# Optimization experiments

Measured on AMD Instinct MI355X. Metric: run time of the kernel, lower is better.

Reference implementation:

```python
import jax, jax.numpy as jnp
import numpy as np

B, T, C, E = 16, 1024, 256, 512
NUM_CENTER = [512, 256, 128]
NUM_NNS = [16, 32, 64]
BN_EPS = 1e-5


def _fps(pts, K):
    # farthest point sampling, deterministic start at index 0. pts: [B,N,3] -> [B,K] int32
    N = pts.shape[1]
    def one(p):
        def step(carry, _):
            d, cur = carry
            dist = jnp.sum((p - p[cur]) ** 2, axis=-1)
            d = jnp.minimum(d, dist)
            nxt = jnp.argmax(d).astype(jnp.int32)
            return (d, nxt), cur
        init = (jnp.full((N,), jnp.inf, p.dtype), jnp.int32(0))
        _, idxs = jax.lax.scan(step, init, None, length=K)
        return idxs
    return jax.vmap(one)(pts)


def _knn(q, t, k):
    # k nearest neighbors of each query q [B,Tq,3] among targets t [B,Tt,3] -> [B,Tq,k]
    d2 = (jnp.sum(q * q, -1)[:, :, None] + jnp.sum(t * t, -1)[:, None, :]
          - 2.0 * jnp.einsum('bqc,btc->bqt', q, t))
    _, idx = jax.lax.top_k(-d2, k)
    return idx


def _gather(x, idx):
    # x [B,N,C], idx [B,M] -> [B,M,C]
    return jax.vmap(lambda xb, ib: xb[ib])(x, idx)


def _knn_gather(x, idx):
    # x [B,N,C], idx [B,M,K] -> [B,M,K,C]
    return jax.vmap(lambda xb, ib: xb[ib])(x, idx)


def _bn(x, g, b):
    # training-mode BatchNorm1d over leading (batch) dim of [N,C]
    m = jnp.mean(x, axis=0)
    v = jnp.mean((x - m) ** 2, axis=0)
    return (x - m) * jax.lax.rsqrt(v + BN_EPS) * g + b


def reference(tokens, centers, lrfs, wq, wkv, mlp_w1, mlp_b1, mlp_w2, mlp_b2,
              bn1_g, bn1_b, bn2_g, bn2_b, att_w1, att_b1, att_w2, att_b2,
              emb_w, emb_b, embn_g, embn_b):
    Bq, Tt, Cd = tokens.shape
    centers_target = centers
    lrfs_target = lrfs.reshape(Bq, Tt, 9)
    tokens_target = tokens
    T_target = Tt
    for i in range(len(NUM_CENTER)):
        Tq = NUM_CENTER[i]
        k = NUM_NNS[i]
        rep_idx = _fps(centers_target, Tq)                      # [B,Tq]
        centers_query = _gather(centers_target, rep_idx)        # [B,Tq,3]
        lrfs_query = _gather(lrfs_target, rep_idx)              # [B,Tq,9]
        tokens_query = _gather(tokens_target, rep_idx)          # [B,Tq,C]
        nn_idx = _knn(centers_query, centers_target, k)         # [B,Tq,k]
        skip = tokens_query.reshape(Bq * Tq, Cd)
        if i > 0:
            t = jnp.concatenate([tokens_query, tokens_target], axis=1)
            t = _bn(t.reshape(Bq * (Tq + T_target), Cd), bn1_g[i], bn1_b[i])
            t = t.reshape(Bq, Tq + T_target, Cd)
            tokens_query, tokens_target = t[:, :Tq, :], t[:, Tq:, :]
        Q = tokens_query @ wq[i]                                # [B,Tq,C]
        KV = tokens_target @ wkv[i]                             # [B,Tt,2C]
        Kf, Vf = KV[..., :Cd], KV[..., Cd:]
        Kn = _knn_gather(Kf, nn_idx).reshape(Bq * Tq, k, Cd)
        Vn = _knn_gather(Vf, nn_idx).reshape(Bq * Tq, k, Cd)
        Qf = Q.reshape(Bq * Tq, Cd)
        # vector self-attention: elementwise Q-K diff -> MLP -> softmax over neighbors
        diff = Qf[:, None, :] - Kn                              # [B*Tq,k,C]
        sim = jax.nn.relu(diff @ att_w1[i] + att_b1[i]) @ att_w2[i] + att_b2[i]
        A = jax.nn.softmax(sim, axis=1)
        tq = jnp.sum(A * Vn, axis=1)                            # [B*Tq,C]
        tq = tq + skip
        skip2 = tq
        tq = _bn(tq, bn2_g[i], bn2_b[i])
        tq = jax.nn.relu(tq @ mlp_w1[i] + mlp_b1[i]) @ mlp_w2[i] + mlp_b2[i]
        tq = tq + skip2
        T_target = Tq
        centers_target = centers_query
        lrfs_target = lrfs_query
        tokens_target = tq.reshape(Bq, Tq, Cd)
    g = jnp.mean(tokens_target, axis=1)                         # [B,C]
    g = jax.nn.relu(_bn(g @ emb_w + emb_b, embn_g, embn_b))     # [B,E]
    # ksparse: keep top-64 activations per row
    vals, _ = jax.lax.top_k(g, 64)
    thr = vals[:, -1:]
    g = jnp.where(g >= thr, g, 0.0)
    n = jnp.maximum(jnp.linalg.norm(g, axis=1, keepdims=True), 1e-12)
    return g / n


def setup_inputs() -> dict:
    key = jax.random.key(0)
    ks = jax.random.split(key, 10)
    s = 0.05
    return {
        'tokens': jax.random.normal(ks[0], (B, T, C), jnp.float32),
        'centers': jax.random.normal(ks[1], (B, T, 3), jnp.float32),
        'lrfs': jax.random.normal(ks[2], (B, T, 3, 3), jnp.float32),
        'wq': jax.random.normal(ks[3], (3, C, C), jnp.float32) * s,
        'wkv': jax.random.normal(ks[4], (3, C, 2 * C), jnp.float32) * s,
        'mlp_w1': jax.random.normal(ks[5], (3, C, 2 * C), jnp.float32) * s,
        'mlp_b1': jnp.zeros((3, 2 * C), jnp.float32),
        'mlp_w2': jax.random.normal(ks[6], (3, 2 * C, C), jnp.float32) * s,
        'mlp_b2': jnp.zeros((3, C), jnp.float32),
        'bn1_g': jnp.ones((3, C), jnp.float32),
        'bn1_b': jnp.zeros((3, C), jnp.float32),
        'bn2_g': jnp.ones((3, C), jnp.float32),
        'bn2_b': jnp.zeros((3, C), jnp.float32),
        'att_w1': jax.random.normal(ks[7], (3, C, C), jnp.float32) * s,
        'att_b1': jnp.zeros((3, C), jnp.float32),
        'att_w2': jax.random.normal(ks[8], (3, C, C), jnp.float32) * s,
        'att_b2': jnp.zeros((3, C), jnp.float32),
        'emb_w': jax.random.normal(ks[9], (C, E), jnp.float32) * s,
        'emb_b': jnp.zeros((E,), jnp.float32),
        'embn_g': jnp.ones((E,), jnp.float32),
        'embn_b': jnp.zeros((E,), jnp.float32),
    }
```

## Files before the change

### kernel.cpp

```cpp
#include <hip/hip_runtime.h>
#include <cstdint>
#include <cmath>

static constexpr int BB = 16;
static constexpr int TT0 = 1024;
static constexpr int CC = 256;
static constexpr int EE = 512;

typedef __bf16 bf16x8 __attribute__((ext_vector_type(8)));
typedef float  f32x4  __attribute__((ext_vector_type(4)));

template <int NPL>
__device__ void fps_body(float4* sp, const float* __restrict__ ctr,
                         int Tt, int Ksel, int* __restrict__ rep,
                         int b, int lane)
{
  const float* base = ctr + (size_t)b * Tt * 3;
  float x[NPL], y[NPL], z[NPL], d[NPL];
  #pragma unroll
  for (int j = 0; j < NPL; ++j) {
    int idx = lane * NPL + j;
    x[j] = base[idx * 3 + 0];
    y[j] = base[idx * 3 + 1];
    z[j] = base[idx * 3 + 2];
    d[j] = INFINITY;
    sp[idx] = make_float4(x[j], y[j], z[j], 0.f);
  }
  int cur = 0;
  for (int s = 0; s < Ksel; ++s) {
    if (lane == 0) rep[b * Ksel + s] = cur;
    float4 cpt = sp[cur];
    unsigned long long key = 0ull;
    #pragma unroll
    for (int j = 0; j < NPL; ++j) {
      float dx = __fsub_rn(x[j], cpt.x);
      float dy = __fsub_rn(y[j], cpt.y);
      float dz = __fsub_rn(z[j], cpt.z);
      float dist = __fadd_rn(__fadd_rn(__fmul_rn(dx, dx), __fmul_rn(dy, dy)),
                             __fmul_rn(dz, dz));
      float nd = fminf(d[j], dist);
      d[j] = nd;
      unsigned long long kj =
          ((unsigned long long)__float_as_uint(nd) << 32) |
          (unsigned)(0xFFFFFFFFu - (unsigned)(lane * NPL + j));
      key = (kj > key) ? kj : key;
    }
    float ld = __uint_as_float((unsigned)(key >> 32));
    float rm = ld;
    {
      int t;
      t = __builtin_amdgcn_mov_dpp(__float_as_int(rm), 0x121, 0xf, 0xf, false);
      rm = fmaxf(rm, __int_as_float(t));
      t = __builtin_amdgcn_mov_dpp(__float_as_int(rm), 0x122, 0xf, 0xf, false);
      rm = fmaxf(rm, __int_as_float(t));
      t = __builtin_amdgcn_mov_dpp(__float_as_int(rm), 0x124, 0xf, 0xf, false);
      rm = fmaxf(rm, __int_as_float(t));
      t = __builtin_amdgcn_mov_dpp(__float_as_int(rm), 0x128, 0xf, 0xf, false);
      rm = fmaxf(rm, __int_as_float(t));
    }
    float r0 = __uint_as_float((unsigned)__builtin_amdgcn_readlane(__float_as_int(rm), 0));
    float r1 = __uint_as_float((unsigned)__builtin_amdgcn_readlane(__float_as_int(rm), 16));
    float r2 = __uint_as_float((unsigned)__builtin_amdgcn_readlane(__float_as_int(rm), 32));
    float r3 = __uint_as_float((unsigned)__builtin_amdgcn_readlane(__float_as_int(rm), 48));
    float gm = fmaxf(fmaxf(r0, r1), fmaxf(r2, r3));
    unsigned long long mask = __ballot(ld == gm);
    int wl = __ffsll(mask) - 1;
    unsigned lowkey = (unsigned)__builtin_amdgcn_readlane((int)(unsigned)key, wl);
    cur = (int)(0xFFFFFFFFu - lowkey);
  }
}

template <int NPL2>
__global__ __launch_bounds__(256) void knn_wave_kernel(
    const float* __restrict__ cq, const float* __restrict__ ct,
    int Tq, int Tt, int Kn, int* __restrict__ nn)
{
  int wid = threadIdx.x >> 6, lane = threadIdx.x & 63;
  int r = blockIdx.x * 4 + wid;
  int b = r / Tq;
  const float* tb = ct + (size_t)b * Tt * 3;
  float qx = cq[(size_t)r * 3 + 0];
  float qy = cq[(size_t)r * 3 + 1];
  float qz = cq[(size_t)r * 3 + 2];
  float sq = __fadd_rn(__fadd_rn(__fmul_rn(qx, qx), __fmul_rn(qy, qy)),
                       __fmul_rn(qz, qz));
  unsigned long long key[NPL2];
  #pragma unroll
  for (int j = 0; j < NPL2; ++j) {
    int t = lane * NPL2 + j;
    float tx = tb[t * 3 + 0], ty = tb[t * 3 + 1], tz = tb[t * 3 + 2];
    float st = __fadd_rn(__fadd_rn(__fmul_rn(tx, tx), __fmul_rn(ty, ty)),
                         __fmul_rn(tz, tz));
    float dot = __fadd_rn(__fadd_rn(__fmul_rn(qx, tx), __fmul_rn(qy, ty)),
                          __fmul_rn(qz, tz));
    float d2 = __fsub_rn(__fadd_rn(sq, st), __fmul_rn(2.0f, dot));
    unsigned ub = __float_as_uint(d2);
    ub ^= (ub >> 31) ? 0xFFFFFFFFu : 0x80000000u;
    key[j] = ((unsigned long long)ub << 32) | (unsigned)t;
  }
  for (int k = 0; k < Kn; ++k) {
    unsigned long long lmin = ~0ull;
    #pragma unroll
    for (int j = 0; j < NPL2; ++j) lmin = (key[j] < lmin) ? key[j] : lmin;
    unsigned md = (unsigned)(lmin >> 32);
    unsigned rm = md;
    {
      unsigned t;
      t = (unsigned)__builtin_amdgcn_mov_dpp((int)rm, 0x121, 0xf, 0xf, false);
      rm = (t < rm) ? t : rm;
      t = (unsigned)__builtin_amdgcn_mov_dpp((int)rm, 0x122, 0xf, 0xf, false);
      rm = (t < rm) ? t : rm;
      t = (unsigned)__builtin_amdgcn_mov_dpp((int)rm, 0x124, 0xf, 0xf, false);
      rm = (t < rm) ? t : rm;
      t = (unsigned)__builtin_amdgcn_mov_dpp((int)rm, 0x128, 0xf, 0xf, false);
      rm = (t < rm) ? t : rm;
    }
    unsigned r0 = (unsigned)__builtin_amdgcn_readlane((int)rm, 0);
    unsigned r1 = (unsigned)__builtin_amdgcn_readlane((int)rm, 16);
    unsigned r2 = (unsigned)__builtin_amdgcn_readlane((int)rm, 32);
    unsigned r3 = (unsigned)__builtin_amdgcn_readlane((int)rm, 48);
    unsigned g01 = (r0 < r1) ? r0 : r1;
    unsigned g23 = (r2 < r3) ? r2 : r3;
    unsigned gmin = (g01 < g23) ? g01 : g23;
    unsigned long long mask = __ballot(md == gmin);
    int wl = __ffsll(mask) - 1;
    int wt = __builtin_amdgcn_readlane((int)(unsigned)lmin, wl);
    if (lane == 0) nn[(size_t)r * Kn + k] = wt;
    #pragma unroll
    for (int j = 0; j < NPL2; ++j)
      if (lane * NPL2 + j == wt) key[j] = ~0ull;
  }
}

__global__ void gather_rows_kernel(
    const float* __restrict__ src, const int* __restrict__ idx,
    float* __restrict__ dst, int Tq, int Tt, int D, int total)
{
  int i = blockIdx.x * blockDim.x + threadIdx.x;
  if (i >= total) return;
  int d = i % D;
  int q = (i / D) % Tq;
  int b = i / (D * Tq);
  int s = idx[b * Tq + q];
  dst[i] = src[((size_t)b * Tt + s) * D + d];
}

__global__ __launch_bounds__(256) void bn_stats_kernel(
    const float* __restrict__ x1, int R1, const float* __restrict__ x2, int R2,
    float* __restrict__ part, int nch)
{
  int c = threadIdx.x;
  int chunk = blockIdx.x;
  int R = R1 + R2;
  int per = (R + nch - 1) / nch;
  int r0 = chunk * per;
  int r1 = min(r0 + per, R);
  float s = 0.f, ss = 0.f;
  for (int r = r0; r < r1; ++r) {
    float v = (r < R1) ? x1[(size_t)r * 256 + c] : x2[(size_t)(r - R1) * 256 + c];
    s += v;
    ss = fmaf(v, v, ss);
  }
  part[(size_t)chunk * 512 + c] = s;
  part[(size_t)chunk * 512 + 256 + c] = ss;
}

__global__ __launch_bounds__(256) void bn_finalize_kernel(
    const float* __restrict__ part, int nch, int R,
    float* __restrict__ mean, float* __restrict__ rstd)
{
  int c = threadIdx.x;
  float s = 0.f, ss = 0.f;
  for (int k = 0; k < nch; ++k) {
    s += part[(size_t)k * 512 + c];
    ss += part[(size_t)k * 512 + 256 + c];
  }
  float m = s / (float)R;
  float v = ss / (float)R - m * m;
  if (v < 0.f) v = 0.f;
  mean[c] = m;
  rstd[c] = rsqrtf(v + 1e-5f);
}

__global__ __launch_bounds__(256) void gemm_kernel(
    const float* __restrict__ A, int lda,
    const float* __restrict__ W, int ldw,
    const float* __restrict__ bias, const float* __restrict__ resid,
    float* __restrict__ out, int M, int N, int K, int relu)
{
  __shared__ float As[32][68];
  __shared__ float Bs[32][68];
  int bm = blockIdx.y * 64;
  int bn = blockIdx.x * 64;
  int tid = threadIdx.x;
  int tx = tid & 15, ty = tid >> 4;
  int arow = tid >> 3;
  int ak = (tid & 7) * 4;
  int wk = tid >> 4;
  int wn = (tid & 15) * 4;
  float acc[4][4] = {{0.f}};
  for (int k0 = 0; k0 < K; k0 += 32) {
    #pragma unroll
    for (int h = 0; h < 2; ++h) {
      int row = bm + arow + h * 32;
      float4 a = (row < M)
          ? *(const float4*)&A[(size_t)row * lda + k0 + ak]
          : make_float4(0.f, 0.f, 0.f, 0.f);
      As[ak + 0][arow + h * 32] = a.x;
      As[ak + 1][arow + h * 32] = a.y;
      As[ak + 2][arow + h * 32] = a.z;
      As[ak + 3][arow + h * 32] = a.w;
    }
    #pragma unroll
    for (int h = 0; h < 2; ++h) {
      int krow = k0 + wk + h * 16;
      *(float4*)&Bs[wk + h * 16][wn] =
          *(const float4*)&W[(size_t)krow * ldw + bn + wn];
    }
    __syncthreads();
    #pragma unroll
    for (int k = 0; k < 32; ++k) {
      float4 a = *(const float4*)&As[k][ty * 4];
      float4 b = *(const float4*)&Bs[k][tx * 4];
      float av[4] = {a.x, a.y, a.z, a.w};
      float bv[4] = {b.x, b.y, b.z, b.w};
      #pragma unroll
      for (int i = 0; i < 4; ++i)
        #pragma unroll
        for (int j = 0; j < 4; ++j)
          acc[i][j] = fmaf(av[i], bv[j], acc[i][j]);
    }
    __syncthreads();
  }
  #pragma unroll
  for (int i = 0; i < 4; ++i) {
    int m = bm + ty * 4 + i;
    if (m >= M) continue;
    #pragma unroll
    for (int j = 0; j < 4; ++j) {
      int n = bn + tx * 4 + j;
      float v = acc[i][j];
      if (bias) v += bias[n];
      if (relu) v = fmaxf(v, 0.f);
      if (resid) v += resid[(size_t)m * N + n];
      out[(size_t)m * N + n] = v;
    }
  }
}

__global__ void splitT_kernel(
    const float* __restrict__ src, int ldw, int K, int N,
    __bf16* __restrict__ hi, __bf16* __restrict__ lo, int total)
{
  int i = blockIdx.x * blockDim.x + threadIdx.x;
  if (i >= total) return;
  int n = i / K;
  int k = i - n * K;
  float v = src[(size_t)k * ldw + n];
  __bf16 h = (__bf16)v;
  hi[i] = h;
  lo[i] = (__bf16)(v - (float)h);
}

__global__ __launch_bounds__(256) void split_w2_kernel(
    const float* __restrict__ w2, __bf16* __restrict__ hi,
    __bf16* __restrict__ lo)
{
  int i = blockIdx.x * 256 + threadIdx.x;
  int s = i >> 16;
  int e = i & 65535;
  int cp = e >> 8;
  int cc = e & 255;
  float v = w2[((size_t)s << 16) + cc * 256 + cp];
  __bf16 h = (__bf16)v;
  hi[i] = h;
  lo[i] = (__bf16)(v - (float)h);
}

template <int NPL>
__global__ __launch_bounds__(256) void gemm_mfma_kernel(
    const float* __restrict__ A, int lda,
    const __bf16* __restrict__ WThi, const __bf16* __restrict__ WTlo,
    const float* __restrict__ bias, const float* __restrict__ resid,
    float* __restrict__ out, int M, int N, int K, int relu,
    const float* __restrict__ bnm, const float* __restrict__ bnr,
    const float* __restrict__ bng, const float* __restrict__ bnb,
    int nbx,
    const float* __restrict__ fps_ctr, int fps_Tt, int fps_Ksel,
    int* __restrict__ fps_rep)
{
  __shared__ __align__(16) float As[128 * 36];
  if ((int)blockIdx.x >= nbx) {
    if (fps_rep == nullptr || (int)blockIdx.y >= BB) return;
    if ((int)threadIdx.x >= 64) return;
    fps_body<NPL>((float4*)As, fps_ctr, fps_Tt, fps_Ksel, fps_rep,
                  blockIdx.y, threadIdx.x);
    return;
  }
  int bm = blockIdx.y * 128;
  int bn = blockIdx.x * 64;
  int tid = threadIdx.x;
  int w = tid >> 6, lane = tid & 63;
  int jl = lane & 15;
  int kg = lane >> 4;

  f32x4 acc[2][4];
  #pragma unroll
  for (int mt = 0; mt < 2; ++mt)
    #pragma unroll
    for (int nt = 0; nt < 4; ++nt) acc[mt][nt] = (f32x4){0.f, 0.f, 0.f, 0.f};

  for (int k0 = 0; k0 < K; k0 += 32) {
    #pragma unroll
    for (int f = 0; f < 4; ++f) {
      int fi = tid + f * 256;
      int row = fi >> 3, c4 = fi & 7;
      float4 v = *(const float4*)&A[(size_t)(bm + row) * lda + k0 + c4 * 4];
      if (bnm) {
        int kk = k0 + c4 * 4;
        float4 m4 = *(const float4*)&bnm[kk];
        float4 r4 = *(const float4*)&bnr[kk];
        float4 g4 = *(const float4*)&bng[kk];
        float4 b4 = *(const float4*)&bnb[kk];
        v.x = (v.x - m4.x) * r4.x * g4.x + b4.x;
        v.y = (v.y - m4.y) * r4.y * g4.y + b4.y;
        v.z = (v.z - m4.z) * r4.z * g4.z + b4.z;
        v.w = (v.w - m4.w) * r4.w * g4.w + b4.w;
      }
      *(float4*)&As[row * 36 + c4 * 4] = v;
    }
    __syncthreads();
    bf16x8 ahi[2], alo[2];
    #pragma unroll
    for (int mt = 0; mt < 2; ++mt) {
      int row = (w * 2 + mt) * 16 + jl;
      float4 a0 = *(const float4*)&As[row * 36 + kg * 8];
      float4 a1 = *(const float4*)&As[row * 36 + kg * 8 + 4];
      float hv[8] = {a0.x, a0.y, a0.z, a0.w, a1.x, a1.y, a1.z, a1.w};
      #pragma unroll
      for (int i = 0; i < 8; ++i) {
        __bf16 t0 = (__bf16)hv[i];
        ahi[mt][i] = t0;
        alo[mt][i] = (__bf16)(hv[i] - (float)t0);
      }
    }
    #pragma unroll
    for (int nt = 0; nt < 4; ++nt) {
      size_t boff = (size_t)(bn + nt * 16 + jl) * K + k0 + kg * 8;
      bf16x8 bhi = *(const bf16x8*)(WThi + boff);
      bf16x8 blo = *(const bf16x8*)(WTlo + boff);
      #pragma unroll
      for (int mt = 0; mt < 2; ++mt) {
        acc[mt][nt] = __builtin_amdgcn_mfma_f32_16x16x32_bf16(alo[mt], bhi, acc[mt][nt], 0, 0, 0);
        acc[mt][nt] = __builtin_amdgcn_mfma_f32_16x16x32_bf16(ahi[mt], blo, acc[mt][nt], 0, 0, 0);
        acc[mt][nt] = __builtin_amdgcn_mfma_f32_16x16x32_bf16(ahi[mt], bhi, acc[mt][nt], 0, 0, 0);
      }
    }
    __syncthreads();
  }
  #pragma unroll
  for (int mt = 0; mt < 2; ++mt)
    #pragma unroll
    for (int nt = 0; nt < 4; ++nt)
      #pragma unroll
      for (int qi = 0; qi < 4; ++qi) {
        int m = bm + (w * 2 + mt) * 16 + kg * 4 + qi;
        int n = bn + nt * 16 + jl;
        float v = acc[mt][nt][qi];
        if (bias) v += bias[n];
        if (relu) v = fmaxf(v, 0.f);
        if (resid) v += resid[(size_t)m * N + n];
        out[(size_t)m * N + n] = v;
      }
}

template <int KN>
__global__ __launch_bounds__(256, 2) void attn5_kernel(
    const float* __restrict__ Qw, const float* __restrict__ KV,
    const int* __restrict__ nn,
    const float* __restrict__ b1, const __bf16* __restrict__ w2Thi,
    const __bf16* __restrict__ w2Tlo, const float* __restrict__ b2,
    const float* __restrict__ skip, float* __restrict__ out, int Tq, int Tt)
{
  constexpr int G  = 128 / KN;
  constexpr int GC = 64 / KN;
  constexpr int LD = 260;
  __shared__ float sim[64 * LD];
  __shared__ int nns[128];
  int r0 = blockIdx.x * G;
  int b = r0 / Tq;
  int tid = threadIdx.x;
  if (tid < 128) nns[tid] = nn[(size_t)r0 * KN + tid];
  __syncthreads();

  int w = tid >> 6, lane = tid & 63;
  int jl = lane & 15;
  int kg = lane >> 4;
  int nt0 = w * 4;
  const float* kvb = KV + (size_t)b * Tt * 512;

  f32x4 acc[8][4];
  #pragma unroll
  for (int m = 0; m < 8; ++m)
    #pragma unroll
    for (int n = 0; n < 4; ++n) acc[m][n] = (f32x4){0.f, 0.f, 0.f, 0.f};

  const float* qp[8];
  const float* kp[8];
  #pragma unroll
  for (int mt = 0; mt < 8; ++mt) {
    int jr = mt * 16 + jl;
    qp[mt] = Qw + (size_t)(r0 + jr / KN) * 256;
    kp[mt] = kvb + (size_t)nns[jr] * 512;
  }

  #pragma unroll
  for (int ks = 0; ks < 8; ++ks) {
    int c0 = ks * 32 + kg * 8;
    float4 b1a = *(const float4*)(b1 + c0);
    float4 b1b = *(const float4*)(b1 + c0 + 4);
    bf16x8 ahi[8], alo[8];
    #pragma unroll
    for (int mt = 0; mt < 8; ++mt) {
      float4 qa = *(const float4*)(qp[mt] + c0);
      float4 qb = *(const float4*)(qp[mt] + c0 + 4);
      float4 ka = *(const float4*)(kp[mt] + c0);
      float4 kb = *(const float4*)(kp[mt] + c0 + 4);
      float h[8];
      h[0] = fmaxf(qa.x - ka.x + b1a.x, 0.f);
      h[1] = fmaxf(qa.y - ka.y + b1a.y, 0.f);
      h[2] = fmaxf(qa.z - ka.z + b1a.z, 0.f);
      h[3] = fmaxf(qa.w - ka.w + b1a.w, 0.f);
      h[4] = fmaxf(qb.x - kb.x + b1b.x, 0.f);
      h[5] = fmaxf(qb.y - kb.y + b1b.y, 0.f);
      h[6] = fmaxf(qb.z - kb.z + b1b.z, 0.f);
      h[7] = fmaxf(qb.w - kb.w + b1b.w, 0.f);
      #pragma unroll
      for (int i = 0; i < 8; ++i) {
        __bf16 t0 = (__bf16)h[i];
        ahi[mt][i] = t0;
        alo[mt][i] = (__bf16)(h[i] - (float)t0);
      }
    }
    #pragma unroll
    for (int t = 0; t < 4; ++t) {
      size_t boff = (size_t)((nt0 + t) * 16 + jl) * 256 + c0;
      bf16x8 bhi = *(const bf16x8*)(w2Thi + boff);
      bf16x8 blo = *(const bf16x8*)(w2Tlo + boff);
      #pragma unroll
      for (int mt = 0; mt < 8; ++mt) {
        acc[mt][t] = __builtin_amdgcn_mfma_f32_16x16x32_bf16(alo[mt], bhi, acc[mt][t], 0, 0, 0);
        acc[mt][t] = __builtin_amdgcn_mfma_f32_16x16x32_bf16(ahi[mt], blo, acc[mt][t], 0, 0, 0);
        acc[mt][t] = __builtin_amdgcn_mfma_f32_16x16x32_bf16(ahi[mt], bhi, acc[mt][t], 0, 0, 0);
      }
    }
  }

  int c = tid;
  float bb2 = b2[c];
  const float* vbb = kvb + 256;
  #pragma unroll
  for (int ch = 0; ch < 2; ++ch) {
    if (ch) __syncthreads();
    #pragma unroll
    for (int m2 = 0; m2 < 4; ++m2) {
      int mt = ch * 4 + m2;
      #pragma unroll
      for (int t = 0; t < 4; ++t)
        #pragma unroll
        for (int qi = 0; qi < 4; ++qi)
          sim[(m2 * 16 + kg * 4 + qi) * LD + (nt0 + t) * 16 + jl] = acc[mt][t][qi];
    }
    __syncthreads();
    #pragma unroll
    for (int gg = 0; gg < GC; ++gg) {
      int jb_l = gg * KN;
      int jb_g = ch * 64 + gg * KN;
      float m = -INFINITY;
      #pragma unroll 8
      for (int jj = 0; jj < KN; ++jj)
        m = fmaxf(m, sim[(jb_l + jj) * LD + c] + bb2);
      float ssum = 0.f, o = 0.f;
      #pragma unroll 8
      for (int jj = 0; jj < KN; ++jj) {
        float e = expf(sim[(jb_l + jj) * LD + c] + bb2 - m);
        ssum += e;
        o = fmaf(e, vbb[(size_t)nns[jb_g + jj] * 512 + c], o);
      }
      int r = r0 + ch * GC + gg;
      out[(size_t)r * 256 + c] = o / ssum + skip[(size_t)r * 256 + c];
    }
  }
}

__global__ void gmean_kernel(const float* __restrict__ tok,
                             float* __restrict__ out, int Tt)
{
  int i = blockIdx.x * blockDim.x + threadIdx.x;
  if (i >= BB * CC) return;
  int b = i >> 8;
  int c = i & 255;
  float s = 0.f;
  for (int t = 0; t < Tt; ++t) s += tok[((size_t)b * Tt + t) * 256 + c];
  out[i] = s / (float)Tt;
}

__global__ void embbn_kernel(const float* __restrict__ x,
                             const float* __restrict__ g,
                             const float* __restrict__ bta,
                             float* __restrict__ y)
{
  int e = blockIdx.x * blockDim.x + threadIdx.x;
  if (e >= EE) return;
  float s = 0.f;
  for (int r = 0; r < BB; ++r) s += x[r * EE + e];
  float m = s / (float)BB;
  float vs = 0.f;
  for (int r = 0; r < BB; ++r) {
    float d = x[r * EE + e] - m;
    vs = fmaf(d, d, vs);
  }
  float rs = rsqrtf(vs / (float)BB + 1e-5f);
  for (int r = 0; r < BB; ++r) {
    float val = (x[r * EE + e] - m) * rs * g[e] + bta[e];
    y[r * EE + e] = fmaxf(val, 0.f);
  }
}

__global__ __launch_bounds__(256) void topk_norm_kernel(
    const float* __restrict__ gin, float* __restrict__ out)
{
  int b = blockIdx.x, tid = threadIdx.x, lane = tid & 63, wid = tid >> 6;
  __shared__ float vals[512];
  __shared__ float wv[4];
  __shared__ int wi[4];
  __shared__ float sh;
  float g0 = gin[b * 512 + tid];
  float g1 = gin[b * 512 + 256 + tid];
  vals[tid] = g0;
  vals[256 + tid] = g1;
  __syncthreads();
  for (int it = 0; it < 64; ++it) {
    float v = vals[tid];
    int ix = tid;
    float u = vals[256 + tid];
    if (u > v) { v = u; ix = 256 + tid; }
    #pragma unroll
    for (int off = 32; off > 0; off >>= 1) {
      float ov = __shfl_down(v, off);
      int oi = __shfl_down(ix, off);
      if (ov > v || (ov == v && oi < ix)) { v = ov; ix = oi; }
    }
    if (lane == 0) { wv[wid] = v; wi[wid] = ix; }
    __syncthreads();
    if (tid == 0) {
      float bv = wv[0]; int bi = wi[0];
      for (int w = 1; w < 4; ++w)
        if (wv[w] > bv || (wv[w] == bv && wi[w] < bi)) { bv = wv[w]; bi = wi[w]; }
      vals[bi] = -INFINITY;
      sh = bv;
    }
    __syncthreads();
  }
  float thr = sh;
  float m0 = (g0 >= thr) ? g0 : 0.f;
  float m1 = (g1 >= thr) ? g1 : 0.f;
  float ss = m0 * m0 + m1 * m1;
  #pragma unroll
  for (int off = 32; off > 0; off >>= 1) ss += __shfl_down(ss, off);
  if (lane == 0) wv[wid] = ss;
  __syncthreads();
  if (tid == 0) {
    float t = wv[0] + wv[1] + wv[2] + wv[3];
    sh = fmaxf(sqrtf(t), 1e-12f);
  }
  __syncthreads();
  float n = sh;
  out[b * 512 + tid] = m0 / n;
  out[b * 512 + 256 + tid] = m1 / n;
}

extern "C" void kernel_launch(void* const* d_in, const int* in_sizes, int n_in,
                              void* d_out, int out_size, void* d_ws, size_t ws_size,
                              hipStream_t stream)
{
  const float* tokens  = (const float*)d_in[0];
  const float* centers = (const float*)d_in[1];
  const float* wq      = (const float*)d_in[3];
  const float* wkv     = (const float*)d_in[4];
  const float* mlp_w1  = (const float*)d_in[5];
  const float* mlp_b1  = (const float*)d_in[6];
  const float* mlp_w2  = (const float*)d_in[7];
  const float* mlp_b2  = (const float*)d_in[8];
  const float* bn1_g   = (const float*)d_in[9];
  const float* bn1_b   = (const float*)d_in[10];
  const float* bn2_g   = (const float*)d_in[11];
  const float* bn2_b   = (const float*)d_in[12];
  const float* att_w1  = (const float*)d_in[13];
  const float* att_b1  = (const float*)d_in[14];
  const float* att_w2  = (const float*)d_in[15];
  const float* att_b2  = (const float*)d_in[16];
  const float* emb_w   = (const float*)d_in[17];
  const float* emb_b   = (const float*)d_in[18];
  const float* embn_g  = (const float*)d_in[19];
  const float* embn_b  = (const float*)d_in[20];
  (void)in_sizes; (void)n_in; (void)out_size; (void)ws_size;

  char* ws = (char*)d_ws;
  size_t off = 0;
  auto alloc = [&](size_t bytes) -> void* {
    void* p = ws + off;
    off += (bytes + 255) & ~(size_t)255;
    return p;
  };
  const size_t tokMax  = (size_t)BB * 512 * CC * 4;
  float* tokA     = (float*)alloc(tokMax);
  float* tokB     = (float*)alloc(tokMax);
  float* ctrA     = (float*)alloc((size_t)BB * 512 * 3 * 4);
  float* ctrB     = (float*)alloc((size_t)BB * 256 * 3 * 4);
  float* ctrC     = (float*)alloc((size_t)BB * 128 * 3 * 4);
  float* tokq_raw = (float*)alloc(tokMax);
  float* Qw1      = (float*)alloc(tokMax);
  float* KVbuf    = (float*)alloc((size_t)BB * 1024 * 512 * 4);
  float* tq1      = (float*)alloc(tokMax);
  float* mlph     = (float*)alloc((size_t)BB * 512 * 512 * 4);
  float* WFq      = (float*)alloc((size_t)3 * CC * CC * 4);
  float* WFk      = (float*)alloc((size_t)3 * CC * CC * 4);
  __bf16* w2Thi   = (__bf16*)alloc((size_t)3 * CC * CC * 2);
  __bf16* w2Tlo   = (__bf16*)alloc((size_t)3 * CC * CC * 2);
  __bf16* wfqThi  = (__bf16*)alloc((size_t)3 * CC * CC * 2);
  __bf16* wfqTlo  = (__bf16*)alloc((size_t)3 * CC * CC * 2);
  __bf16* wkvThi  = (__bf16*)alloc((size_t)3 * 512 * CC * 2);
  __bf16* wkvTlo  = (__bf16*)alloc((size_t)3 * 512 * CC * 2);
  __bf16* w1Thi   = (__bf16*)alloc((size_t)3 * CC * 512 * 2);
  __bf16* w1Tlo   = (__bf16*)alloc((size_t)3 * CC * 512 * 2);
  __bf16* wm2Thi  = (__bf16*)alloc((size_t)3 * 512 * CC * 2);
  __bf16* wm2Tlo  = (__bf16*)alloc((size_t)3 * 512 * CC * 2);
  int*   rep0     = (int*)alloc((size_t)BB * 512 * 4);
  int*   rep1     = (int*)alloc((size_t)BB * 256 * 4);
  int*   rep2     = (int*)alloc((size_t)BB * 128 * 4);
  int*   nnb      = (int*)alloc((size_t)BB * 512 * 64 * 4);
  float* bnpart   = (float*)alloc((size_t)64 * 512 * 4);
  float* bn1mean  = (float*)alloc(256 * 4);
  float* bn1rstd  = (float*)alloc(256 * 4);
  float* bn2mean  = (float*)alloc(256 * 4);
  float* bn2rstd  = (float*)alloc(256 * 4);
  float* gmeanb   = (float*)alloc((size_t)BB * CC * 4);
  float* gembb    = (float*)alloc((size_t)BB * EE * 4);
  float* grelub   = (float*)alloc((size_t)BB * EE * 4);

  const int NC[3] = {512, 256, 128};
  const int NN[3] = {16, 32, 64};
  int* reps[3] = {rep0, rep1, rep2};
  float* ctrq[3] = {ctrA, ctrB, ctrC};

  for (int i = 0; i < 3; ++i) {
    gemm_kernel<<<dim3(4, 4), 256, 0, stream>>>(
        wq + (size_t)i * CC * CC, CC, att_w1 + (size_t)i * CC * CC, CC,
        nullptr, nullptr, WFq + (size_t)i * CC * CC, CC, CC, CC, 0);
    gemm_kernel<<<dim3(4, 4), 256, 0, stream>>>(
        wkv + (size_t)i * CC * 512, 512, att_w1 + (size_t)i * CC * CC, CC,
        nullptr, nullptr, WFk + (size_t)i * CC * CC, CC, CC, CC, 0);
  }
  split_w2_kernel<<<3 * 65536 / 256, 256, 0, stream>>>(att_w2, w2Thi, w2Tlo);
  for (int i = 0; i < 3; ++i) {
    int t1 = CC * CC;
    splitT_kernel<<<(t1 + 255) / 256, 256, 0, stream>>>(
        WFq + (size_t)i * CC * CC, CC, CC, CC,
        wfqThi + (size_t)i * t1, wfqTlo + (size_t)i * t1, t1);
    splitT_kernel<<<(t1 + 255) / 256, 256, 0, stream>>>(
        WFk + (size_t)i * CC * CC, CC, CC, CC,
        wkvThi + (size_t)i * 512 * CC, wkvTlo + (size_t)i * 512 * CC, t1);
    splitT_kernel<<<(t1 + 255) / 256, 256, 0, stream>>>(
        wkv + (size_t)i * CC * 512 + CC, 512, CC, CC,
        wkvThi + (size_t)i * 512 * CC + t1, wkvTlo + (size_t)i * 512 * CC + t1, t1);
    int t2 = CC * 512;
    splitT_kernel<<<(t2 + 255) / 256, 256, 0, stream>>>(
        mlp_w1 + (size_t)i * t2, 512, CC, 512,
        w1Thi + (size_t)i * t2, w1Tlo + (size_t)i * t2, t2);
    splitT_kernel<<<(t2 + 255) / 256, 256, 0, stream>>>(
        mlp_w2 + (size_t)i * t2, CC, 512, CC,
        wm2Thi + (size_t)i * t2, wm2Tlo + (size_t)i * t2, t2);
  }

  const float* cur_tok = tokens;
  const float* cur_ctr = centers;
  int curTt = TT0;
  float* tok_bufs[2] = {tokA, tokB};

  for (int i = 0; i < 3; ++i) {
    int Tq = NC[i], Kn = NN[i], Tt = curTt;
    float* ctr_q = ctrq[i];
    float* tok_next = tok_bufs[i & 1];
    int M = BB * Tq;
    int Mt = BB * Tt;
    int* rep = reps[i];

    const float *b1m = nullptr, *b1r = nullptr, *b1g = nullptr, *b1b = nullptr;

    if (i == 0) {
      gemm_mfma_kernel<16><<<dim3(512 / 64 + 1, Mt / 128), 256, 0, stream>>>(
          tokens, CC, wkvThi, wkvTlo, nullptr, nullptr, KVbuf,
          Mt, 512, CC, 0, nullptr, nullptr, nullptr, nullptr,
          512 / 64, centers, 1024, 512, rep0);
    }

    {
      int tot = BB * Tq * 3;
      gather_rows_kernel<<<(tot + 255) / 256, 256, 0, stream>>>(
          cur_ctr, rep, ctr_q, Tq, Tt, 3, tot);
    }
    {
      int tot = M * CC;
      gather_rows_kernel<<<(tot + 255) / 256, 256, 0, stream>>>(
          cur_tok, rep, tokq_raw, Tq, Tt, CC, tot);
    }
    if (Tt == 1024)
      knn_wave_kernel<16><<<M / 4, 256, 0, stream>>>(ctr_q, cur_ctr, Tq, Tt, Kn, nnb);
    else if (Tt == 512)
      knn_wave_kernel<8><<<M / 4, 256, 0, stream>>>(ctr_q, cur_ctr, Tq, Tt, Kn, nnb);
    else
      knn_wave_kernel<4><<<M / 4, 256, 0, stream>>>(ctr_q, cur_ctr, Tq, Tt, Kn, nnb);

    if (i > 0) {
      bn_stats_kernel<<<64, 256, 0, stream>>>(tokq_raw, M, cur_tok, Mt, bnpart, 64);
      bn_finalize_kernel<<<1, 256, 0, stream>>>(bnpart, 64, M + Mt, bn1mean, bn1rstd);
      b1m = bn1mean; b1r = bn1rstd; b1g = bn1_g + i * CC; b1b = bn1_b + i * CC;
      if (i == 1)
        gemm_mfma_kernel<4><<<dim3(512 / 64 + 1, Mt / 128), 256, 0, stream>>>(
            cur_tok, CC, wkvThi + (size_t)i * 512 * CC, wkvTlo + (size_t)i * 512 * CC,
            nullptr, nullptr, KVbuf, Mt, 512, CC, 0, b1m, b1r, b1g, b1b,
            512 / 64, ctrB, 256, 128, rep2);
      else
        gemm_mfma_kernel<4><<<dim3(512 / 64, Mt / 128), 256, 0, stream>>>(
            cur_tok, CC, wkvThi + (size_t)i * 512 * CC, wkvTlo + (size_t)i * 512 * CC,
            nullptr, nullptr, KVbuf, Mt, 512, CC, 0, b1m, b1r, b1g, b1b,
            512 / 64, nullptr, 0, 0, nullptr);
    }

    gemm_mfma_kernel<4><<<dim3(CC / 64, M / 128), 256, 0, stream>>>(
        tokq_raw, CC, wfqThi + (size_t)i * CC * CC, wfqTlo + (size_t)i * CC * CC,
        nullptr, nullptr, Qw1, M, CC, CC, 0, b1m, b1r, b1g, b1b,
        CC / 64, nullptr, 0, 0, nullptr);

    if (Kn == 16)
      attn5_kernel<16><<<dim3(M / 8), 256, 0, stream>>>(
          Qw1, KVbuf, nnb, att_b1 + i * CC,
          w2Thi + (size_t)i * CC * CC, w2Tlo + (size_t)i * CC * CC,
          att_b2 + i * CC, tokq_raw, tq1, Tq, Tt);
    else if (Kn == 32)
      attn5_kernel<32><<<dim3(M / 4), 256, 0, stream>>>(
          Qw1, KVbuf, nnb, att_b1 + i * CC,
          w2Thi + (size_t)i * CC * CC, w2Tlo + (size_t)i * CC * CC,
          att_b2 + i * CC, tokq_raw, tq1, Tq, Tt);
    else
      attn5_kernel<64><<<dim3(M / 2), 256, 0, stream>>>(
          Qw1, KVbuf, nnb, att_b1 + i * CC,
          w2Thi + (size_t)i * CC * CC, w2Tlo + (size_t)i * CC * CC,
          att_b2 + i * CC, tokq_raw, tq1, Tq, Tt);

    bn_stats_kernel<<<64, 256, 0, stream>>>(tq1, M, tq1, 0, bnpart, 64);
    bn_finalize_kernel<<<1, 256, 0, stream>>>(bnpart, 64, M, bn2mean, bn2rstd);
    if (i == 0)
      gemm_mfma_kernel<8><<<dim3(512 / 64 + 1, M / 128), 256, 0, stream>>>(
          tq1, CC, w1Thi + (size_t)i * CC * 512, w1Tlo + (size_t)i * CC * 512,
          mlp_b1 + i * 512, nullptr, mlph, M, 512, CC, 1,
          bn2mean, bn2rstd, bn2_g + i * CC, bn2_b + i * CC,
          512 / 64, ctrA, 512, 256, rep1);
    else
      gemm_mfma_kernel<4><<<dim3(512 / 64, M / 128), 256, 0, stream>>>(
          tq1, CC, w1Thi + (size_t)i * CC * 512, w1Tlo + (size_t)i * CC * 512,
          mlp_b1 + i * 512, nullptr, mlph, M, 512, CC, 1,
          bn2mean, bn2rstd, bn2_g + i * CC, bn2_b + i * CC,
          512 / 64, nullptr, 0, 0, nullptr);
    gemm_mfma_kernel<4><<<dim3(CC / 64, M / 128), 256, 0, stream>>>(
        mlph, 512, wm2Thi + (size_t)i * 512 * CC, wm2Tlo + (size_t)i * 512 * CC,
        mlp_b2 + i * CC, tq1, tok_next, M, CC, 512, 0,
        nullptr, nullptr, nullptr, nullptr,
        CC / 64, nullptr, 0, 0, nullptr);

    cur_tok = tok_next;
    cur_ctr = ctr_q;
    curTt = Tq;
  }

  gmean_kernel<<<(BB * CC + 255) / 256, 256, 0, stream>>>(cur_tok, gmeanb, curTt);
  gemm_kernel<<<dim3(EE / 64, 1), 256, 0, stream>>>(
      gmeanb, CC, emb_w, EE, emb_b, nullptr, gembb, BB, EE, CC, 0);
  embbn_kernel<<<2, 256, 0, stream>>>(gembb, embn_g, embn_b, grelub);
  topk_norm_kernel<<<BB, 256, 0, stream>>>(grelub, (float*)d_out);
}
```

Baseline: 1.605 ms.

## Overlap next-stage FPS with attention kernel and fuse weight fold with split

```diff
diff --git a/kernel.cpp b/kernel.cpp
--- a/kernel.cpp
+++ b/kernel.cpp
@@ -244,6 +244,67 @@
       if (relu) v = fmaxf(v, 0.f);
       if (resid) v += resid[(size_t)m * N + n];
       out[(size_t)m * N + n] = v;
+    }
+  }
+}
+
+__global__ __launch_bounds__(256) void gemm_fold_split_kernel(
+    const float* __restrict__ A, int lda,
+    const float* __restrict__ W, int ldw,
+    __bf16* __restrict__ hi, __bf16* __restrict__ lo, int M, int N, int K)
+{
+  __shared__ float As[32][68];
+  __shared__ float Bs[32][68];
+  int bm = blockIdx.y * 64;
+  int bn = blockIdx.x * 64;
+  int tid = threadIdx.x;
+  int tx = tid & 15, ty = tid >> 4;
+  int arow = tid >> 3;
+  int ak = (tid & 7) * 4;
+  int wk = tid >> 4;
+  int wn = (tid & 15) * 4;
+  float acc[4][4] = {{0.f}};
+  for (int k0 = 0; k0 < K; k0 += 32) {
+    #pragma unroll
+    for (int h = 0; h < 2; ++h) {
+      int row = bm + arow + h * 32;
+      float4 a = *(const float4*)&A[(size_t)row * lda + k0 + ak];
+      As[ak + 0][arow + h * 32] = a.x;
+      As[ak + 1][arow + h * 32] = a.y;
+      As[ak + 2][arow + h * 32] = a.z;
+      As[ak + 3][arow + h * 32] = a.w;
+    }
+    #pragma unroll
+    for (int h = 0; h < 2; ++h) {
+      int krow = k0 + wk + h * 16;
+      *(float4*)&Bs[wk + h * 16][wn] =
+          *(const float4*)&W[(size_t)krow * ldw + bn + wn];
+    }
+    __syncthreads();
+    #pragma unroll
+    for (int k = 0; k < 32; ++k) {
+      float4 a = *(const float4*)&As[k][ty * 4];
+      float4 b = *(const float4*)&Bs[k][tx * 4];
+      float av[4] = {a.x, a.y, a.z, a.w};
+      float bv[4] = {b.x, b.y, b.z, b.w};
+      #pragma unroll
+      for (int i = 0; i < 4; ++i)
+        #pragma unroll
+        for (int j = 0; j < 4; ++j)
+          acc[i][j] = fmaf(av[i], bv[j], acc[i][j]);
+    }
+    __syncthreads();
+  }
+  #pragma unroll
+  for (int i = 0; i < 4; ++i) {
+    int m = bm + ty * 4 + i;
+    #pragma unroll
+    for (int j = 0; j < 4; ++j) {
+      int n = bn + tx * 4 + j;
+      float v = acc[i][j];
+      __bf16 h = (__bf16)v;
+      hi[(size_t)n * K + m] = h;
+      lo[(size_t)n * K + m] = (__bf16)(v - (float)h);
     }
   }
 }
@@ -374,19 +435,31 @@
       }
 }
 
-template <int KN>
+template <int KN, int NPL>
 __global__ __launch_bounds__(256, 2) void attn5_kernel(
     const float* __restrict__ Qw, const float* __restrict__ KV,
     const int* __restrict__ nn,
     const float* __restrict__ b1, const __bf16* __restrict__ w2Thi,
     const __bf16* __restrict__ w2Tlo, const float* __restrict__ b2,
-    const float* __restrict__ skip, float* __restrict__ out, int Tq, int Tt)
+    const float* __restrict__ skip, float* __restrict__ out, int Tq, int Tt,
+    int nbx,
+    const float* __restrict__ fps_ctr, int fps_Tt, int fps_Ksel,
+    int* __restrict__ fps_rep)
 {
   constexpr int G  = 128 / KN;
   constexpr int GC = 64 / KN;
   constexpr int LD = 260;
-  __shared__ float sim[64 * LD];
+  __shared__ __align__(16) float sim[64 * LD];
   __shared__ int nns[128];
+  if ((int)blockIdx.x >= nbx) {
+    if (fps_rep == nullptr) return;
+    int fb = blockIdx.x - nbx;
+    if (fb >= BB) return;
+    if ((int)threadIdx.x >= 64) return;
+    fps_body<NPL>((float4*)sim, fps_ctr, fps_Tt, fps_Ksel, fps_rep,
+                  fb, threadIdx.x);
+    return;
+  }
   int r0 = blockIdx.x * G;
   int b = r0 / Tq;
   int tid = threadIdx.x;
@@ -624,8 +697,6 @@
   float* KVbuf    = (float*)alloc((size_t)BB * 1024 * 512 * 4);
   float* tq1      = (float*)alloc(tokMax);
   float* mlph     = (float*)alloc((size_t)BB * 512 * 512 * 4);
-  float* WFq      = (float*)alloc((size_t)3 * CC * CC * 4);
-  float* WFk      = (float*)alloc((size_t)3 * CC * CC * 4);
   __bf16* w2Thi   = (__bf16*)alloc((size_t)3 * CC * CC * 2);
   __bf16* w2Tlo   = (__bf16*)alloc((size_t)3 * CC * CC * 2);
   __bf16* wfqThi  = (__bf16*)alloc((size_t)3 * CC * CC * 2);
@@ -655,22 +726,13 @@
   float* ctrq[3] = {ctrA, ctrB, ctrC};
 
   for (int i = 0; i < 3; ++i) {
-    gemm_kernel<<<dim3(4, 4), 256, 0, stream>>>(
+    int t1 = CC * CC;
+    gemm_fold_split_kernel<<<dim3(4, 4), 256, 0, stream>>>(
         wq + (size_t)i * CC * CC, CC, att_w1 + (size_t)i * CC * CC, CC,
-        nullptr, nullptr, WFq + (size_t)i * CC * CC, CC, CC, CC, 0);
-    gemm_kernel<<<dim3(4, 4), 256, 0, stream>>>(
+        wfqThi + (size_t)i * t1, wfqTlo + (size_t)i * t1, CC, CC, CC);
+    gemm_fold_split_kernel<<<dim3(4, 4), 256, 0, stream>>>(
         wkv + (size_t)i * CC * 512, 512, att_w1 + (size_t)i * CC * CC, CC,
-        nullptr, nullptr, WFk + (size_t)i * CC * CC, CC, CC, CC, 0);
-  }
-  split_w2_kernel<<<3 * 65536 / 256, 256, 0, stream>>>(att_w2, w2Thi, w2Tlo);
-  for (int i = 0; i < 3; ++i) {
-    int t1 = CC * CC;
-    splitT_kernel<<<(t1 + 255) / 256, 256, 0, stream>>>(
-        WFq + (size_t)i * CC * CC, CC, CC, CC,
-        wfqThi + (size_t)i * t1, wfqTlo + (size_t)i * t1, t1);
-    splitT_kernel<<<(t1 + 255) / 256, 256, 0, stream>>>(
-        WFk + (size_t)i * CC * CC, CC, CC, CC,
-        wkvThi + (size_t)i * 512 * CC, wkvTlo + (size_t)i * 512 * CC, t1);
+        wkvThi + (size_t)i * 512 * CC, wkvTlo + (size_t)i * 512 * CC, CC, CC, CC);
     splitT_kernel<<<(t1 + 255) / 256, 256, 0, stream>>>(
         wkv + (size_t)i * CC * 512 + CC, 512, CC, CC,
         wkvThi + (size_t)i * 512 * CC + t1, wkvTlo + (size_t)i * 512 * CC + t1, t1);
@@ -682,6 +744,7 @@
         mlp_w2 + (size_t)i * t2, CC, 512, CC,
         wm2Thi + (size_t)i * t2, wm2Tlo + (size_t)i * t2, t2);
   }
+  split_w2_kernel<<<3 * 65536 / 256, 256, 0, stream>>>(att_w2, w2Thi, w2Tlo);
 
   const float* cur_tok = tokens;
   const float* cur_ctr = centers;
@@ -726,16 +789,10 @@
       bn_stats_kernel<<<64, 256, 0, stream>>>(tokq_raw, M, cur_tok, Mt, bnpart, 64);
       bn_finalize_kernel<<<1, 256, 0, stream>>>(bnpart, 64, M + Mt, bn1mean, bn1rstd);
       b1m = bn1mean; b1r = bn1rstd; b1g = bn1_g + i * CC; b1b = bn1_b + i * CC;
-      if (i == 1)
-        gemm_mfma_kernel<4><<<dim3(512 / 64 + 1, Mt / 128), 256, 0, stream>>>(
-            cur_tok, CC, wkvThi + (size_t)i * 512 * CC, wkvTlo + (size_t)i * 512 * CC,
-            nullptr, nullptr, KVbuf, Mt, 512, CC, 0, b1m, b1r, b1g, b1b,
-            512 / 64, ctrB, 256, 128, rep2);
-      else
-        gemm_mfma_kernel<4><<<dim3(512 / 64, Mt / 128), 256, 0, stream>>>(
-            cur_tok, CC, wkvThi + (size_t)i * 512 * CC, wkvTlo + (size_t)i * 512 * CC,
-            nullptr, nullptr, KVbuf, Mt, 512, CC, 0, b1m, b1r, b1g, b1b,
-            512 / 64, nullptr, 0, 0, nullptr);
+      gemm_mfma_kernel<4><<<dim3(512 / 64, Mt / 128), 256, 0, stream>>>(
+          cur_tok, CC, wkvThi + (size_t)i * 512 * CC, wkvTlo + (size_t)i * 512 * CC,
+          nullptr, nullptr, KVbuf, Mt, 512, CC, 0, b1m, b1r, b1g, b1b,
+          512 / 64, nullptr, 0, 0, nullptr);
     }
 
     gemm_mfma_kernel<4><<<dim3(CC / 64, M / 128), 256, 0, stream>>>(
@@ -744,35 +801,31 @@
         CC / 64, nullptr, 0, 0, nullptr);
 
     if (Kn == 16)
-      attn5_kernel<16><<<dim3(M / 8), 256, 0, stream>>>(
+      attn5_kernel<16, 8><<<dim3(M / 8 + 16), 256, 0, stream>>>(
           Qw1, KVbuf, nnb, att_b1 + i * CC,
           w2Thi + (size_t)i * CC * CC, w2Tlo + (size_t)i * CC * CC,
-          att_b2 + i * CC, tokq_raw, tq1, Tq, Tt);
+          att_b2 + i * CC, tokq_raw, tq1, Tq, Tt,
+          M / 8, ctrA, 512, 256, rep1);
     else if (Kn == 32)
-      attn5_kernel<32><<<dim3(M / 4), 256, 0, stream>>>(
+      attn5_kernel<32, 4><<<dim3(M / 4 + 16), 256, 0, stream>>>(
           Qw1, KVbuf, nnb, att_b1 + i * CC,
           w2Thi + (size_t)i * CC * CC, w2Tlo + (size_t)i * CC * CC,
-          att_b2 + i * CC, tokq_raw, tq1, Tq, Tt);
+          att_b2 + i * CC, tokq_raw, tq1, Tq, Tt,
+          M / 4, ctrB, 256, 128, rep2);
     else
-      attn5_kernel<64><<<dim3(M / 2), 256, 0, stream>>>(
+      attn5_kernel<64, 4><<<dim3(M / 2), 256, 0, stream>>>(
           Qw1, KVbuf, nnb, att_b1 + i * CC,
           w2Thi + (size_t)i * CC * CC, w2Tlo + (size_t)i * CC * CC,
-          att_b2 + i * CC, tokq_raw, tq1, Tq, Tt);
+          att_b2 + i * CC, tokq_raw, tq1, Tq, Tt,
+          M / 2, nullptr, 0, 0, nullptr);
 
     bn_stats_kernel<<<64, 256, 0, stream>>>(tq1, M, tq1, 0, bnpart, 64);
     bn_finalize_kernel<<<1, 256, 0, stream>>>(bnpart, 64, M, bn2mean, bn2rstd);
-    if (i == 0)
-      gemm_mfma_kernel<8><<<dim3(512 / 64 + 1, M / 128), 256, 0, stream>>>(
-          tq1, CC, w1Thi + (size_t)i * CC * 512, w1Tlo + (size_t)i * CC * 512,
-          mlp_b1 + i * 512, nullptr, mlph, M, 512, CC, 1,
-          bn2mean, bn2rstd, bn2_g + i * CC, bn2_b + i * CC,
-          512 / 64, ctrA, 512, 256, rep1);
-    else
-      gemm_mfma_kernel<4><<<dim3(512 / 64, M / 128), 256, 0, stream>>>(
-          tq1, CC, w1Thi + (size_t)i * CC * 512, w1Tlo + (size_t)i * CC * 512,
-          mlp_b1 + i * 512, nullptr, mlph, M, 512, CC, 1,
-          bn2mean, bn2rstd, bn2_g + i * CC, bn2_b + i * CC,
-          512 / 64, nullptr, 0, 0, nullptr);
+    gemm_mfma_kernel<4><<<dim3(512 / 64, M / 128), 256, 0, stream>>>(
+        tq1, CC, w1Thi + (size_t)i * CC * 512, w1Tlo + (size_t)i * CC * 512,
+        mlp_b1 + i * 512, nullptr, mlph, M, 512, CC, 1,
+        bn2mean, bn2rstd, bn2_g + i * CC, bn2_b + i * CC,
+        512 / 64, nullptr, 0, 0, nullptr);
     gemm_mfma_kernel<4><<<dim3(CC / 64, M / 128), 256, 0, stream>>>(
         mlph, 512, wm2Thi + (size_t)i * 512 * CC, wm2Tlo + (size_t)i * 512 * CC,
         mlp_b2 + i * CC, tq1, tok_next, M, CC, 512, 0,
```

Measured after the change: 1.638 ms. 1.02x slower.
